# Optimization experiments

Measured on AMD Instinct MI355X. Metric: run time of the kernel, lower is better.

Reference implementation:

```python
import jax, jax.numpy as jnp
import numpy as np
from functools import partial

N_SEEDS = 1000       # n
BG_LOW, BG_UP = 0.3, 0.7
ERODE_K, ERODE_ITER = 11, 1
KSZ = 3
IGNORE = -255
INT_MAX = np.iinfo(np.int32).max


def _min_pool2d(x, k):
    # binary erosion with a kxk all-ones structuring element, SAME padding
    return jax.lax.reduce_window(x, INT_MAX, jax.lax.min, (k, k), (1, 1), 'SAME')


def _max_pool3d(x, k):
    # binary dilation over (B,H,W) with kxk window on spatial dims
    return jax.lax.reduce_window(x, -INT_MAX, jax.lax.max, (1, k, k), (1, 1, 1), 'SAME')


def _otsu_threshold(flat255):
    # flat255: int32 pixel values in [0,255]
    hist = jnp.zeros(256, jnp.float32).at[flat255].add(1.0)
    total = jnp.asarray(flat255.shape[0], jnp.float32)
    bins = jnp.arange(256, dtype=jnp.float32)
    w = jnp.cumsum(hist)                 # class-0 pixel count up to bin t
    m = jnp.cumsum(hist * bins)          # class-0 intensity mass up to t
    mT = m[-1]
    denom = w * (total - w)
    sigma_b = jnp.where(denom > 0, (mT * w - total * m) ** 2 / (denom * total * total), 0.0)
    th = jnp.argmax(sigma_b).astype(jnp.float32)
    bad = jnp.sum(hist > 0) <= 1         # degenerate histogram -> bad_egg
    return th, bad


def _sample_mask(eligible, key, hw):
    # uniform sampling without replacement of min(N_SEEDS, #eligible)
    # via random-score top-k restricted to eligible positions
    scores = jnp.where(eligible, jax.random.uniform(key, (hw,)), -jnp.inf)
    vals, idx = jax.lax.top_k(scores, N_SEEDS)
    sel = (vals > -jnp.inf).astype(jnp.int32)
    return jnp.zeros(hw, jnp.int32).at[idx].max(sel)


def _one_sample(cam, key):
    h, w = cam.shape
    hw = h * w
    cam255 = jnp.floor(cam * 255.0)
    flat255 = jnp.clip(cam255.astype(jnp.int32).ravel(), 0, 255)

    th, bad = _otsu_threshold(flat255)
    th = jnp.where(bad, jnp.median(cam * 255.0), th)
    th = jnp.where(th == 0, 1.0, jnp.where(th == 255, 254.0, th))

    roi = (cam255 > th).astype(jnp.int32)
    for _ in range(ERODE_ITER):
        roi = _min_pool2d(roi, ERODE_K)

    kf, kb, kz = jax.random.split(key, 3)
    # foreground: sample uniformly from eroded ROI pixels
    fg = _sample_mask(roi.ravel() == 1, kf, hw)
    # background: sample uniformly from the nbr_bg lowest-activation pixels
    z = jax.random.uniform(kz, (), minval=BG_LOW, maxval=BG_UP)
    nbr_bg = jnp.ceil(z * hw)
    order = jnp.argsort(cam.ravel())
    rank = jnp.zeros(hw, jnp.int32).at[order].set(jnp.arange(hw, dtype=jnp.int32))
    bg = _sample_mask(rank.astype(jnp.float32) < nbr_bg, kb, hw)
    return fg.reshape(h, w), bg.reshape(h, w)


def setup_inputs() -> dict:
    key = jax.random.key(0)
    x = jax.random.uniform(key, (128, 1, 512, 512), dtype=jnp.float32)
    return {"x": x}


def reference(x):
    b, d, h, w = x.shape
    keys = jax.random.split(jax.random.key(42), b)
    all_fg, all_bg = jax.vmap(_one_sample)(x[:, 0], keys)   # (B,H,W) int32
    # dilation with ksz x ksz ones kernel
    all_fg = _max_pool3d(all_fg, KSZ)
    all_bg = _max_pool3d(all_bg, KSZ)
    outer = all_fg + all_bg
    all_fg = jnp.where(outer == 2, 0, all_fg)
    all_bg = jnp.where(outer == 2, 0, all_bg)
    out = jnp.full((b, h, w), IGNORE, dtype=jnp.int32)
    out = jnp.where(all_fg == 1, 1, out)
    out = jnp.where(all_bg == 1, 0, out)
    return out
```

## Files before the change

### kernel.cpp

```cpp
#include <hip/hip_runtime.h>
#include <cstdint>

typedef unsigned short u16;

constexpr int BATCH = 128;
constexpr int H = 512, W = 512;
constexpr int HW = H * W;
constexpr int WPR = W / 64;
constexpr int WPI = HW / 64;
constexpr int NSEED = 1000;
constexpr int MARGIN = 3000;
constexpr int CAP2 = 4096;
constexpr int CAPS = 1024;
constexpr int LBUF = 2048;
constexpr int NBIN = 4096;

__device__ __forceinline__ uint32_t rotl32(uint32_t v, int d) {
  return (v << d) | (v >> (32 - d));
}

__device__ __forceinline__ void tf2x32(uint32_t k0, uint32_t k1,
                                       uint32_t x0, uint32_t x1,
                                       uint32_t &o0, uint32_t &o1) {
  uint32_t ks2 = k0 ^ k1 ^ 0x1BD11BDAu;
  x0 += k0; x1 += k1;
  x0 += x1; x1 = rotl32(x1, 13); x1 ^= x0;
  x0 += x1; x1 = rotl32(x1, 15); x1 ^= x0;
  x0 += x1; x1 = rotl32(x1, 26); x1 ^= x0;
  x0 += x1; x1 = rotl32(x1, 6);  x1 ^= x0;
  x0 += k1; x1 += ks2 + 1u;
  x0 += x1; x1 = rotl32(x1, 17); x1 ^= x0;
  x0 += x1; x1 = rotl32(x1, 29); x1 ^= x0;
  x0 += x1; x1 = rotl32(x1, 16); x1 ^= x0;
  x0 += x1; x1 = rotl32(x1, 24); x1 ^= x0;
  x0 += ks2; x1 += k0 + 2u;
  x0 += x1; x1 = rotl32(x1, 13); x1 ^= x0;
  x0 += x1; x1 = rotl32(x1, 15); x1 ^= x0;
  x0 += x1; x1 = rotl32(x1, 26); x1 ^= x0;
// ... 23 lines not shown
  uint32_t kf0, kf1; tf2x32(kb0, kb1, 0u, 0u, kf0, kf1);
  uint32_t kB0, kB1; tf2x32(kb0, kb1, 0u, 1u, kB0, kB1);
  uint32_t kz0, kz1; tf2x32(kb0, kb1, 0u, 2u, kz0, kz1);
  uint32_t za, zc; tf2x32(kz0, kz1, 0u, 0u, za, zc);
  uint32_t zb = za ^ zc;
  keys[b * 4 + 0] = kf0; keys[b * 4 + 1] = kf1;
  keys[b * 4 + 2] = kB0; keys[b * 4 + 3] = kB1;
  float uu = __uint_as_float((zb >> 9) | 0x3f800000u) - 1.0f;
  float span = __fsub_rn(0.7f, 0.3f);
  float z = __fadd_rn(__fmul_rn(uu, span), 0.3f);
  z = fmaxf(0.3f, z);
  float nb = ceilf(__fmul_rn(z, (float)HW));
  uint32_t K = (uint32_t)nb;
  kbg[b] = K;
  float tv = floorf((1.0f - (float)MARGIN / (float)K) * 8388608.0f);
  Tbg[b] = (uint32_t)fmaxf(tv, 0.0f);
}

__global__ __launch_bounds__(1024) void k_binify(const float4* __restrict__ x4,
                                                 u16* __restrict__ g,
                                                 uint32_t* __restrict__ gh,
                                                 uint32_t* __restrict__ keys,
                                                 uint32_t* __restrict__ kbg,
                                                 uint32_t* __restrict__ Tbg) {
  __shared__ uint32_t h[NBIN];
  int b = blockIdx.x >> 2, sub = blockIdx.x & 3, t = threadIdx.x;
  if (blockIdx.x == 0 && t < BATCH) keygen(t, keys, kbg, Tbg);
  for (int i = t; i < NBIN; i += 1024) h[i] = 0;
  __syncthreads();
  const float4* xb = x4 + ((size_t)b * HW + (size_t)sub * (HW / 4)) / 4;
  ushort4* gb4 = (ushort4*)g + ((size_t)b * HW + (size_t)sub * (HW / 4)) / 4;
  for (int i = t; i < HW / 16; i += 1024) {
    float4 v4 = xb[i];
    int g0 = (int)floorf(__fmul_rn(v4.x, 4080.0f)); g0 = min(max(g0, 0), 4079);
    int g1 = (int)floorf(__fmul_rn(v4.y, 4080.0f)); g1 = min(max(g1, 0), 4079);
    int g2 = (int)floorf(__fmul_rn(v4.z, 4080.0f)); g2 = min(max(g2, 0), 4079);
    int g3 = (int)floorf(__fmul_rn(v4.w, 4080.0f)); g3 = min(max(g3, 0), 4079);
    atomicAdd(&h[g0], 1u);
    atomicAdd(&h[g1], 1u);
    atomicAdd(&h[g2], 1u);
    atomicAdd(&h[g3], 1u);
    ushort4 o;
    o.x = (u16)g0; o.y = (u16)g1; o.z = (u16)g2; o.w = (u16)g3;
    gb4[i] = o;
  }
  __syncthreads();
  for (int i = t; i < NBIN; i += 1024)
    if (h[i]) atomicAdd(&gh[(size_t)b * NBIN + i], h[i]);
}

__device__ __forceinline__ void lds_tree_cumsum256(float* L, float* S, int tid) {
  const int off[9] = {0, 256, 384, 448, 480, 496, 504, 508, 510};
  const int sz[9]  = {256, 128, 64, 32, 16, 8, 4, 2, 1};
  for (int l = 0; l < 8; ++l) {
    int o = off[l], on = off[l + 1], n = sz[l + 1];
    if (tid < n) L[on + tid] = __fadd_rn(L[o + 2 * tid], L[o + 2 * tid + 1]);
    __syncthreads();
  }
  if (tid == 0) S[off[8]] = L[off[8]];
  __syncthreads();
  for (int l = 7; l >= 0; --l) {
    int o = off[l], on = off[l + 1], hn = sz[l] / 2;
    if (tid == 0) S[o] = L[o];
    if (tid < hn) S[o + 2 * tid + 1] = S[on + tid];
    if (tid >= 1 && tid < hn) S[o + 2 * tid] = __fadd_rn(S[on + tid - 1], L[o + 2 * tid]);
    __syncthreads();
  }
}

__global__ __launch_bounds__(256) void k_otsu_scan(const uint32_t* __restrict__ gh,
                                                   const uint32_t* __restrict__ Ka,
                                                   int* __restrict__ th_out,
                                                   uint32_t* __restrict__ b1a,
                                                   uint32_t* __restrict__ r1a) {
  __shared__ float L[511], S[511], wc[256], mm[256];
  __shared__ float sv[256];
  __shared__ int si[256];
  __shared__ uint32_t h[NBIN];
  __shared__ uint32_t ps[256];
  int tid = threadIdx.x;
  if (blockIdx.x < BATCH) {
    int b = blockIdx.x;
    const uint32_t* gg = gh + (size_t)b * NBIN;
    for (int i = tid; i < NBIN; i += 256) h[i] = gg[i];
    __syncthreads();
    uint32_t hv = 0;
#pragma unroll
    for (int i = 0; i < 16; ++i) hv += h[tid * 16 + i];
    L[tid] = (float)hv;
    __syncthreads();
    lds_tree_cumsum256(L, S, tid);
    wc[tid] = S[tid];
    __syncthreads();
    L[tid] = __fmul_rn((float)hv, (float)tid);
    __syncthreads();
    lds_tree_cumsum256(L, S, tid);
    mm[tid] = S[tid];
    __syncthreads();
    float total = (float)HW;
    float mT = mm[255];
    {
      float w = wc[tid];
      float denom = __fmul_rn(w, __fsub_rn(total, w));
      float s = 0.0f;
      if (denom > 0.0f) {
        float d  = __fsub_rn(__fmul_rn(mT, w), __fmul_rn(total, mm[tid]));
        float nu = __fmul_rn(d, d);
        float dd = __fmul_rn(__fmul_rn(denom, total), total);
        s = __fdiv_rn(nu, dd);
      }
      sv[tid] = s; si[tid] = tid;
    }
    __syncthreads();
    for (int st = 128; st >= 1; st >>= 1) {
      if (tid < st) {
        float s2 = sv[tid + st]; int i2 = si[tid + st];
        if (s2 > sv[tid] || (s2 == sv[tid] && i2 < si[tid])) { sv[tid] = s2; si[tid] = i2; }
      }
      __syncthreads();
    }
    if (tid == 0) {
      int bi = si[0];
      if (bi == 0) bi = 1;
      if (bi == 255) bi = 254;
      th_out[b] = bi;
    }
  } else {
    int b = blockIdx.x - BATCH;
    uint32_t K = Ka[b];
    const uint32_t* g = gh + (size_t)b * NBIN;
    for (int i = tid; i < NBIN; i += 256) h[i] = g[i];
    __syncthreads();
    uint32_t s = 0;
#pragma unroll
    for (int i = 0; i < 16; ++i) s += h[tid * 16 + i];
    ps[tid] = s;
    __syncthreads();
    if (tid == 0) {
      uint32_t acc = 0, b1 = 0, r1 = 1;
      for (int c = 0; c < 256; ++c) {
        if (acc + ps[c] >= K) {
          for (int bin = c * 16; bin < c * 16 + 16; ++bin) {
            uint32_t cc = h[bin];
            if (acc + cc >= K) { b1 = (uint32_t)bin; r1 = K - acc; break; }
            acc += cc;
          }
          break;
        }
        acc += ps[c];
      }
      b1a[b] = b1; r1a[b] = r1;
    }
  }
}

__global__ __launch_bounds__(1024) void k_main(const u16* __restrict__ gq,
                                               const float* __restrict__ x,
                                               const int* __restrict__ th,
                                               const uint32_t* __restrict__ b1a,
                                               const uint32_t* __restrict__ Tbg,
                                               const uint32_t* __restrict__ keys,
                                               uint32_t* __restrict__ Efg,
                                               uint32_t* __restrict__ cnt_bg,
                                               uint64_t* __restrict__ list,
                                               uint32_t* __restrict__ cnt_be,
                                               uint64_t* __restrict__ list_be,
                                               uint64_t* __restrict__ erod) {
  __shared__ uint64_t sroi[1104];
  __shared__ uint64_t srow[1104];
  __shared__ uint32_t queue[8192];
  __shared__ uint64_t lbuf[LBUF];
  __shared__ uint32_t qcnt, lcnt, gbase;
  int b = blockIdx.x >> 2, sub = blockIdx.x & 3, t = threadIdx.x;
  int wave = t >> 6, lane = t & 63;
  int R0 = sub * 128;
  int rlo = max(R0 - 5, 0), rhi = min(R0 + 133, H);
  int nrows = rhi - rlo;
  int nwords = nrows * 8;
  const u16* gb = gq + (size_t)b * HW;
  const float* xb = x + (size_t)b * HW;
  int groi = (th[b] + 1) << 4;
  uint32_t b1 = b1a[b];
  uint32_t T = Tbg[b];
  uint32_t k0 = keys[b * 4 + 2], k1 = keys[b * 4 + 3];
  if (t == 0) lcnt = 0;
  __syncthreads();
  int ntiles = (nwords + 127) / 128;
  for (int tile = 0; tile < ntiles; ++tile) {
    if (t == 0) qcnt = 0;
    __syncthreads();
    int wbeg = tile * 128, wend = min(wbeg + 128, nwords);
    for (int wi = wbeg + wave; wi < wend; wi += 16) {
      int srow_i = wi >> 3, c = wi & 7;
      int absr = rlo + srow_i;
      int p = absr * W + c * 64 + lane;
      uint32_t gv = (uint32_t)gb[p];
      bool pred = (int)gv >= groi;
      uint64_t bw = __ballot(pred);
      if (lane == 0) sroi[wi] = bw;
      if (absr >= R0 && absr < R0 + 128) {
        bool elig = gv < b1;
        uint64_t m = __ballot(elig);
        uint32_t base = 0;
        if (lane == 0 && m) base = atomicAdd(&qcnt, (uint32_t)__popcll(m));
        base = (uint32_t)__shfl((int)base, 0);
        if (elig) {
          uint32_t rank = (uint32_t)__popcll(m & ((1ull << lane) - 1ull));
          queue[base + rank] = (uint32_t)p;
        }
        if (gv == b1) {
          uint32_t gp = atomicAdd(&cnt_be[b], 1u);
          if (gp < (uint32_t)CAPS) {
            float v = xb[p];
            list_be[(size_t)b * CAPS + gp] =
                (((uint64_t)__float_as_uint(v)) << 18) | (uint32_t)p;
          }
        }
      }
    }
    __syncthreads();
    uint32_t qn = qcnt;
    for (uint32_t i = t; i < qn; i += 1024) {
      uint32_t p = queue[i];
      uint32_t v = score_bits(k0, k1, p) >> 9;
      if (v >= T) {
        uint32_t pos = atomicAdd(&lcnt, 1u);
        uint64_t key = (((uint64_t)((~v) & 0x7FFFFFu)) << 18) | p;
        if (pos < (uint32_t)LBUF) lbuf[pos] = key;
        else { uint32_t gp = atomicAdd(&cnt_bg[b], 1u);
               if (gp < (uint32_t)CAP2) list[(size_t)b * CAP2 + gp] = key; }
      }
    }
    __syncthreads();
  }
  for (int wi = t; wi < nwords; wi += 1024) {
    int c = wi & 7;
    uint64_t cur = sroi[wi];
    uint64_t left  = (c > 0) ? sroi[wi - 1] : ~0ull;
    uint64_t right = (c < 7) ? sroi[wi + 1] : ~0ull;
    uint64_t res = cur;
#pragma unroll
    for (int s = 1; s <= 5; ++s) {
      res &= (cur >> s) | (right << (64 - s));
      res &= (cur << s) | (left >> (64 - s));
    }
    srow[wi] = res;
  }
  __syncthreads();
  {
    int coreRow = t >> 3, c = t & 7;
    int absr = R0 + coreRow;
    int s = absr - rlo;
    uint64_t res = srow[s * 8 + c];
#pragma unroll
    for (int d = 1; d <= 5; ++d) {
      if (absr - d >= 0) res &= srow[(s - d) * 8 + c];
      if (absr + d < H)  res &= srow[(s + d) * 8 + c];
    }
    erod[(size_t)b * WPI + absr * 8 + c] = res;
    uint32_t pc = (uint32_t)__popcll(res);
    for (int sh = 32; sh >= 1; sh >>= 1) pc += __shfl_down(pc, sh);
    if (lane == 0 && pc) atomicAdd(&Efg[b], pc);
  }
  __syncthreads();
  int m = min((int)lcnt, LBUF);
  if (t == 0) gbase = atomicAdd(&cnt_bg[b], (uint32_t)m);
  __syncthreads();
  uint32_t base = gbase;
  for (int i = t; i < m; i += 1024) {
    uint32_t pos = base + (uint32_t)i;
    if (pos < (uint32_t)CAP2) list[(size_t)b * CAP2 + pos] = lbuf[i];
  }
}

__global__ __launch_bounds__(1024) void k_bgsel(const uint32_t* __restrict__ r1a,
                                                const uint32_t* __restrict__ cnt_be,
                                                const uint64_t* __restrict__ list_be,
                                                const uint32_t* __restrict__ Tbg,
                                                const uint32_t* __restrict__ keys,
                                                const uint32_t* __restrict__ cnt_bg,
                                                const uint64_t* __restrict__ list,
                                                uint64_t* __restrict__ bm) {
  __shared__ uint64_t ks[CAPS];
  __shared__ uint64_t ebuf[CAPS];
  __shared__ uint32_t ecnt;
  __shared__ uint32_t h[4096];
  __shared__ uint32_t S[256];
  __shared__ uint32_t sb2, sr2;
  __shared__ uint64_t tie[1024];
  __shared__ uint32_t tcnt;
  int b = blockIdx.x, t = threadIdx.x;
  int nbe = min((int)cnt_be[b], CAPS);
  if (t == 0) { ecnt = 0; tcnt = 0; }
  if (t < nbe) ks[t] = list_be[(size_t)b * CAPS + t];
  __syncthreads();
  if (t < nbe) {
    uint64_t mk = ks[t];
    int rank = 0;
    for (int i = 0; i < nbe; ++i) rank += (ks[i] < mk) ? 1 : 0;
    int r = min((int)r1a[b], nbe);
    if (rank < r) {
      uint32_t p = (uint32_t)(mk & 0x3FFFFull);
      uint32_t v = score_bits(keys[b * 4 + 2], keys[b * 4 + 3], p) >> 9;
      if (v >= Tbg[b]) {
        uint32_t slot = atomicAdd(&ecnt, 1u);
        ebuf[slot] = (((uint64_t)((~v) & 0x7FFFFFu)) << 18) | p;
      }
    }
  }
  for (int i = t; i < 4096; i += 1024) h[i] = 0;
  __syncthreads();
  int n0 = min((int)cnt_bg[b], CAP2);
  int ne = (int)ecnt;
  int n = n0 + ne;
  if (n == 0) return;
  uint32_t target = (uint32_t)min(NSEED, n);
  const uint64_t* lb = list + (size_t)b * CAP2;
  uint64_t K0 = (t < n0)        ? lb[t]        : 0;
  uint64_t K1 = (t + 1024 < n0) ? lb[t + 1024] : 0;
  uint64_t K2 = (t + 2048 < n0) ? lb[t + 2048] : 0;
  uint64_t K3 = (t + 3072 < n0) ? lb[t + 3072] : 0;
  uint64_t KE = (t < ne)        ? ebuf[t]      : 0;
  if (t < n0)        atomicAdd(&h[(uint32_t)(K0 >> 29)], 1u);
  if (t + 1024 < n0) atomicAdd(&h[(uint32_t)(K1 >> 29)], 1u);
  if (t + 2048 < n0) atomicAdd(&h[(uint32_t)(K2 >> 29)], 1u);
  if (t + 3072 < n0) atomicAdd(&h[(uint32_t)(K3 >> 29)], 1u);
  if (t < ne)        atomicAdd(&h[(uint32_t)(KE >> 29)], 1u);
  __syncthreads();
  if (t < 256) {
    uint32_t s = 0;
#pragma unroll
    for (int i = 0; i < 16; ++i) s += h[t * 16 + i];
    S[t] = s;
  }
  __syncthreads();
  for (int st = 1; st < 256; st <<= 1) {
    uint32_t v = 0;
    if (t < 256 && t >= st) v = S[t - st];
    __syncthreads();
    if (t < 256) S[t] += v;
    __syncthreads();
  }
  if (t < 256) {
    uint32_t before = (t == 0) ? 0u : S[t - 1];
    if (S[t] >= target && before < target) {
      uint32_t acc = before;
      for (int i = 0; i < 16; ++i) {
        uint32_t c = h[t * 16 + i];
        if (acc + c >= target) { sb2 = (uint32_t)(t * 16 + i); sr2 = target - acc; break; }
        acc += c;
      }
    }
  }
  __syncthreads();
  uint32_t b2 = sb2, r2 = sr2;
#define PROC(KK, VALID) \
  if (VALID) { \
    uint32_t bin = (uint32_t)((KK) >> 29); \
    if (bin < b2) { \
      uint32_t p = (uint32_t)(KK) & 0x3FFFFu; \
      atomicOr((unsigned long long*)&bm[(size_t)b * WPI + (p >> 6)], 1ull << (p & 63)); \
    } else if (bin == b2) { \
      uint32_t pos = atomicAdd(&tcnt, 1u); \
      if (pos < 1024u) tie[pos] = (KK); \
    } \
  }
  PROC(K0, t < n0) PROC(K1, t + 1024 < n0) PROC(K2, t + 2048 < n0)
  PROC(K3, t + 3072 < n0) PROC(KE, t < ne)
#undef PROC
  __syncthreads();
  int m = min((int)tcnt, 1024);
  int r = min((int)r2, m);
  if (t < m) {
    uint64_t mk = tie[t];
    int rank = 0;
    for (int i = 0; i < m; ++i) rank += (tie[i] < mk) ? 1 : 0;
    if (rank < r) {
      uint32_t p = (uint32_t)mk & 0x3FFFFu;
      atomicOr((unsigned long long*)&bm[(size_t)b * WPI + (p >> 6)], 1ull << (p & 63));
    }
  }
}

__global__ __launch_bounds__(1024) void k_selfg(const uint64_t* __restrict__ elig,
                                                const uint32_t* __restrict__ keys,
                                                const uint32_t* __restrict__ Ea,
                                                uint32_t* __restrict__ cnt,
                                                uint64_t* __restrict__ list,
                                                uint64_t* __restrict__ out) {
  __shared__ uint64_t lbuf[LBUF];
  __shared__ uint32_t lcnt;
  __shared__ uint32_t gbase;
  int b = blockIdx.x >> 2, sub = blockIdx.x & 3, t = threadIdx.x;
  const uint64_t* eb = elig + (size_t)b * WPI;
  uint64_t* ob = out + (size_t)b * WPI;
  uint32_t E = Ea[b];
  int wbase = sub * (WPI / 4);
  if (E <= (uint32_t)NSEED) {
    for (int w = t; w < WPI / 4; w += 1024) ob[wbase + w] = eb[wbase + w];
    return;
  }
  float tvf = floorf((1.0f - (float)MARGIN / (float)E) * 8388608.0f);
  uint32_t T = (uint32_t)fmaxf(tvf, 0.0f);
  if (t == 0) lcnt = 0;
  for (int w = t; w < WPI / 4; w += 1024) ob[wbase + w] = 0;
  __syncthreads();
  uint32_t k0 = keys[b * 4 + 0], k1 = keys[b * 4 + 1];
  uint32_t pbase = (uint32_t)(sub * (HW / 4));
  for (int i = t; i < HW / 4; i += 2048) {
    uint32_t p1 = pbase + (uint32_t)i;
    uint32_t p2 = p1 + 1024u;
    uint32_t v1 = score_bits(k0, k1, p1) >> 9;
    uint32_t v2 = score_bits(k0, k1, p2) >> 9;
    bool e1 = (eb[p1 >> 6] >> (p1 & 63)) & 1ull;
    bool e2 = (eb[p2 >> 6] >> (p2 & 63)) & 1ull;
    if (e1 && v1 >= T) {
      uint32_t pos = atomicAdd(&lcnt, 1u);
      uint64_t key = (((uint64_t)((~v1) & 0x7FFFFFu)) << 18) | p1;
      if (pos < (uint32_t)LBUF) lbuf[pos] = key;
      else { uint32_t gp = atomicAdd(&cnt[b], 1u);
             if (gp < (uint32_t)CAP2) list[(size_t)b * CAP2 + gp] = key; }
    }
    if (e2 && v2 >= T) {
      uint32_t pos = atomicAdd(&lcnt, 1u);
      uint64_t key = (((uint64_t)((~v2) & 0x7FFFFFu)) << 18) | p2;
      if (pos < (uint32_t)LBUF) lbuf[pos] = key;
      else { uint32_t gp = atomicAdd(&cnt[b], 1u);
             if (gp < (uint32_t)CAP2) list[(size_t)b * CAP2 + gp] = key; }
    }
  }
  __syncthreads();
  int m = min((int)lcnt, LBUF);
  if (t == 0) gbase = atomicAdd(&cnt[b], (uint32_t)m);
  __syncthreads();
  uint32_t base = gbase;
  for (int i = t; i < m; i += 1024) {
    uint32_t pos = base + (uint32_t)i;
    if (pos < (uint32_t)CAP2) list[(size_t)b * CAP2 + pos] = lbuf[i];
  }
}

__global__ __launch_bounds__(1024) void k_cut2xl(const uint32_t* __restrict__ Ea,
                                                 const uint32_t* __restrict__ cnt,
                                                 const uint64_t* __restrict__ list,
                                                 uint64_t* __restrict__ bm) {
  __shared__ uint32_t h[4096];
  __shared__ uint32_t S[256];
  __shared__ uint32_t sb2, sr2;
  __shared__ uint64_t tie[1024];
  __shared__ uint32_t tcnt;
  int b = blockIdx.x, t = threadIdx.x;
  if (Ea[b] <= (uint32_t)NSEED) return;
  int n = min((int)cnt[b], CAP2);
  if (n == 0) return;
  uint32_t target = (uint32_t)min(NSEED, n);
  const uint64_t* lb = list + (size_t)b * CAP2;
  uint64_t K0 = (t < n)        ? lb[t]        : 0;
  uint64_t K1 = (t + 1024 < n) ? lb[t + 1024] : 0;
  uint64_t K2 = (t + 2048 < n) ? lb[t + 2048] : 0;
  uint64_t K3 = (t + 3072 < n) ? lb[t + 3072] : 0;
  for (int i = t; i < 4096; i += 1024) h[i] = 0;
  if (t == 0) tcnt = 0;
  __syncthreads();
  if (t < n)        atomicAdd(&h[(uint32_t)(K0 >> 29)], 1u);
  if (t + 1024 < n) atomicAdd(&h[(uint32_t)(K1 >> 29)], 1u);
  if (t + 2048 < n) atomicAdd(&h[(uint32_t)(K2 >> 29)], 1u);
  if (t + 3072 < n) atomicAdd(&h[(uint32_t)(K3 >> 29)], 1u);
  __syncthreads();
  if (t < 256) {
    uint32_t s = 0;
#pragma unroll
    for (int i = 0; i < 16; ++i) s += h[t * 16 + i];
    S[t] = s;
  }
  __syncthreads();
  for (int st = 1; st < 256; st <<= 1) {
    uint32_t v = 0;
    if (t < 256 && t >= st) v = S[t - st];
    __syncthreads();
    if (t < 256) S[t] += v;
    __syncthreads();
  }
  if (t < 256) {
    uint32_t before = (t == 0) ? 0u : S[t - 1];
    if (S[t] >= target && before < target) {
      uint32_t acc = before;
      for (int i = 0; i < 16; ++i) {
        uint32_t c = h[t * 16 + i];
        if (acc + c >= target) { sb2 = (uint32_t)(t * 16 + i); sr2 = target - acc; break; }
        acc += c;
      }
    }
  }
  __syncthreads();
  uint32_t b2 = sb2, r2 = sr2;
#define PROC(KK, VALID) \
  if (VALID) { \
    uint32_t bin = (uint32_t)((KK) >> 29); \
    if (bin < b2) { \
      uint32_t p = (uint32_t)(KK) & 0x3FFFFu; \
      atomicOr((unsigned long long*)&bm[(size_t)b * WPI + (p >> 6)], 1ull << (p & 63)); \
    } else if (bin == b2) { \
      uint32_t pos = atomicAdd(&tcnt, 1u); \
      if (pos < 1024u) tie[pos] = (KK); \
    } \
  }
  PROC(K0, t < n) PROC(K1, t + 1024 < n) PROC(K2, t + 2048 < n) PROC(K3, t + 3072 < n)
#undef PROC
  __syncthreads();
  int m = min((int)tcnt, 1024);
  int r = min((int)r2, m);
  if (t < m) {
    uint64_t mk = tie[t];
    int rank = 0;
    for (int i = 0; i < m; ++i) rank += (tie[i] < mk) ? 1 : 0;
    if (rank < r) {
      uint32_t p = (uint32_t)mk & 0x3FFFFu;
      atomicOr((unsigned long long*)&bm[(size_t)b * WPI + (p >> 6)], 1ull << (p & 63));
    }
  }
}

__global__ __launch_bounds__(256) void k_compose4(const uint64_t* __restrict__ F,
                                                  const uint64_t* __restrict__ G,
                                                  int* __restrict__ out) {
  int tid = blockIdx.x * 256 + threadIdx.x;
  int w = tid >> 4;
  int sub = tid & 15;
  int iw = w & (WPI - 1);
  int r = iw >> 3, c = iw & 7;
  int ib = w - iw;
  uint64_t Fd = 0, Bd = 0;
#pragma unroll
  for (int dr = -1; dr <= 1; ++dr) {
    int rr = r + dr;
    if (rr < 0 || rr >= H) continue;
    int wi = ib + rr * 8 + c;
    uint64_t cf = F[wi], cg = G[wi];
    uint64_t lf = (c > 0) ? F[wi - 1] : 0ull, lg = (c > 0) ? G[wi - 1] : 0ull;
    uint64_t rf = (c < 7) ? F[wi + 1] : 0ull, rg = (c < 7) ? G[wi + 1] : 0ull;
    Fd |= cf | (cf << 1) | (lf >> 63) | (cf >> 1) | (rf << 63);
    Bd |= cg | (cg << 1) | (lg >> 63) | (cg >> 1) | (rg << 63);
  }
  uint64_t ov = Fd & Bd;
  Fd &= ~ov; Bd &= ~ov;
  int sh = sub * 4;
  int4 o;
  o.x = ((Fd >> (sh + 0)) & 1ull) ? 1 : (((Bd >> (sh + 0)) & 1ull) ? 0 : -255);
  o.y = ((Fd >> (sh + 1)) & 1ull) ? 1 : (((Bd >> (sh + 1)) & 1ull) ? 0 : -255);
  o.z = ((Fd >> (sh + 2)) & 1ull) ? 1 : (((Bd >> (sh + 2)) & 1ull) ? 0 : -255);
  o.w = ((Fd >> (sh + 3)) & 1ull) ? 1 : (((Bd >> (sh + 3)) & 1ull) ? 0 : -255);
  ((int4*)out)[tid] = o;
}

extern "C" void kernel_launch(void* const* d_in, const int* in_sizes, int n_in,
                              void* d_out, int out_size, void* d_ws, size_t ws_size,
                              hipStream_t stream) {
  (void)in_sizes; (void)n_in; (void)out_size; (void)ws_size;
  const float* x = (const float*)d_in[0];
  int* out = (int*)d_out;
  char* ws = (char*)d_ws;

  u16* g = (u16*)d_out;

  uint32_t* keys = (uint32_t*)(ws + 0);
  uint32_t* kbg  = (uint32_t*)(ws + 2048);
  int*      th   = (int*)     (ws + 2560);
  uint32_t* b1be = (uint32_t*)(ws + 3072);
  uint32_t* r1be = (uint32_t*)(ws + 3584);
  uint32_t* Tbg  = (uint32_t*)(ws + 4096);
  char* Z = ws + 8192;
  uint32_t* Efg    = (uint32_t*)(Z + 0);
  uint32_t* cnt_fg = (uint32_t*)(Z + 512);
  uint32_t* cnt_be = (uint32_t*)(Z + 1024);
  uint32_t* cnt_bg = (uint32_t*)(Z + 1536);
  uint32_t* gh     = (uint32_t*)(Z + 2048);
  uint64_t* bmG    = (uint64_t*)(Z + 2048 + 2097152);
  size_t Zsize = 2048 + 2097152 + 4194304;
  char* P = Z + Zsize;
  uint64_t* list    = (uint64_t*)(P + 0);
  uint64_t* list_be = (uint64_t*)(P + 4194304);
  uint64_t* bmE     = (uint64_t*)(P + 5242880);
  uint64_t* bmF     = (uint64_t*)(P + 9437184);

  hipMemsetAsync(Z, 0, Zsize, stream);
  k_binify   <<<BATCH * 4, 1024, 0, stream>>>((const float4*)x, g, gh, keys, kbg, Tbg);
  k_otsu_scan<<<BATCH * 2, 256, 0, stream>>>(gh, kbg, th, b1be, r1be);
  k_main     <<<BATCH * 4, 1024, 0, stream>>>(g, x, th, b1be, Tbg, keys,
                                              Efg, cnt_bg, list, cnt_be, list_be, bmE);
  k_bgsel    <<<BATCH, 1024, 0, stream>>>(r1be, cnt_be, list_be, Tbg, keys,
                                          cnt_bg, list, bmG);
  k_selfg    <<<BATCH * 4, 1024, 0, stream>>>(bmE, keys, Efg, cnt_fg, list, bmF);
  k_cut2xl   <<<BATCH, 1024, 0, stream>>>(Efg, cnt_fg, list, bmF);
  k_compose4 <<<(BATCH * HW / 4) / 256, 256, 0, stream>>>(bmF, bmG, out);
}
```

Baseline: 416.1 us.

## Fuse selection kernels, drop memset, use per-wave ring queues in main

Replaces the workspace memset by zeroing counters in the binify kernel and writing per-block histograms that the Otsu kernel sums. In k_main the block-wide tiled queue with __syncthreads becomes per-wave ring buffers with only wave barriers. The background-select, foreground-select and tie-cut kernels merge into one k_select launch with one role per block, and compose picks the eroded mask directly when the foreground is small. This cuts launches, the memset and block syncs, but the foreground path now runs one block per image instead of four, which lowers parallelism for that part.

```diff
diff --git a/kernel.cpp b/kernel.cpp
--- a/kernel.cpp
+++ b/kernel.cpp
@@ -14,6 +14,7 @@
 constexpr int CAPS = 1024;
 constexpr int LBUF = 2048;
 constexpr int NBIN = 4096;
+constexpr int QSEG = 576;
 
 __device__ __forceinline__ uint32_t rotl32(uint32_t v, int d) {
   return (v << d) | (v >> (32 - d));
@@ -83,10 +84,17 @@
                                                  uint32_t* __restrict__ gh,
                                                  uint32_t* __restrict__ keys,
                                                  uint32_t* __restrict__ kbg,
-                                                 uint32_t* __restrict__ Tbg) {
+                                                 uint32_t* __restrict__ Tbg,
+                                                 uint32_t* __restrict__ Efg,
+                                                 uint32_t* __restrict__ cnt_fg,
+                                                 uint32_t* __restrict__ cnt_be,
+                                                 uint32_t* __restrict__ cnt_bg) {
   __shared__ uint32_t h[NBIN];
   int b = blockIdx.x >> 2, sub = blockIdx.x & 3, t = threadIdx.x;
-  if (blockIdx.x == 0 && t < BATCH) keygen(t, keys, kbg, Tbg);
+  if (blockIdx.x == 0 && t < BATCH) {
+    keygen(t, keys, kbg, Tbg);
+    Efg[t] = 0; cnt_fg[t] = 0; cnt_be[t] = 0; cnt_bg[t] = 0;
+  }
   for (int i = t; i < NBIN; i += 1024) h[i] = 0;
   __syncthreads();
   const float4* xb = x4 + ((size_t)b * HW + (size_t)sub * (HW / 4)) / 4;
@@ -106,8 +114,8 @@
     gb4[i] = o;
   }
   __syncthreads();
-  for (int i = t; i < NBIN; i += 1024)
-    if (h[i]) atomicAdd(&gh[(size_t)b * NBIN + i], h[i]);
+  uint32_t* dst = gh + ((size_t)blockIdx.x << 12);
+  for (int i = t; i < NBIN; i += 1024) dst[i] = h[i];
 }
 
 __device__ __forceinline__ void lds_tree_cumsum256(float* L, float* S, int tid) {
@@ -140,11 +148,14 @@
   __shared__ uint32_t h[NBIN];
   __shared__ uint32_t ps[256];
   int tid = threadIdx.x;
+  int b = (blockIdx.x < BATCH) ? blockIdx.x : (blockIdx.x - BATCH);
+  const uint32_t* g0 = gh + ((size_t)(b * 4 + 0) << 12);
+  const uint32_t* g1 = gh + ((size_t)(b * 4 + 1) << 12);
+  const uint32_t* g2 = gh + ((size_t)(b * 4 + 2) << 12);
+  const uint32_t* g3 = gh + ((size_t)(b * 4 + 3) << 12);
+  for (int i = tid; i < NBIN; i += 256) h[i] = g0[i] + g1[i] + g2[i] + g3[i];
+  __syncthreads();
   if (blockIdx.x < BATCH) {
-    int b = blockIdx.x;
-    const uint32_t* gg = gh + (size_t)b * NBIN;
-    for (int i = tid; i < NBIN; i += 256) h[i] = gg[i];
-    __syncthreads();
     uint32_t hv = 0;
 #pragma unroll
     for (int i = 0; i < 16; ++i) hv += h[tid * 16 + i];
@@ -187,11 +198,7 @@
       th_out[b] = bi;
     }
   } else {
-    int b = blockIdx.x - BATCH;
     uint32_t K = Ka[b];
-    const uint32_t* g = gh + (size_t)b * NBIN;
-    for (int i = tid; i < NBIN; i += 256) h[i] = g[i];
-    __syncthreads();
     uint32_t s = 0;
 #pragma unroll
     for (int i = 0; i < 16; ++i) s += h[tid * 16 + i];
@@ -229,15 +236,14 @@
                                                uint64_t* __restrict__ erod) {
   __shared__ uint64_t sroi[1104];
   __shared__ uint64_t srow[1104];
-  __shared__ uint32_t queue[8192];
+  __shared__ uint32_t wq[16 * QSEG];
   __shared__ uint64_t lbuf[LBUF];
-  __shared__ uint32_t qcnt, lcnt, gbase;
+  __shared__ uint32_t lcnt, gbase;
   int b = blockIdx.x >> 2, sub = blockIdx.x & 3, t = threadIdx.x;
   int wave = t >> 6, lane = t & 63;
   int R0 = sub * 128;
   int rlo = max(R0 - 5, 0), rhi = min(R0 + 133, H);
-  int nrows = rhi - rlo;
-  int nwords = nrows * 8;
+  int nwords = (rhi - rlo) * 8;
   const u16* gb = gq + (size_t)b * HW;
   const float* xb = x + (size_t)b * HW;
   int groi = (th[b] + 1) << 4;
@@ -246,43 +252,46 @@
   uint32_t k0 = keys[b * 4 + 2], k1 = keys[b * 4 + 3];
   if (t == 0) lcnt = 0;
   __syncthreads();
-  int ntiles = (nwords + 127) / 128;
-  for (int tile = 0; tile < ntiles; ++tile) {
-    if (t == 0) qcnt = 0;
-    __syncthreads();
-    int wbeg = tile * 128, wend = min(wbeg + 128, nwords);
-    for (int wi = wbeg + wave; wi < wend; wi += 16) {
-      int srow_i = wi >> 3, c = wi & 7;
-      int absr = rlo + srow_i;
-      int p = absr * W + c * 64 + lane;
-      uint32_t gv = (uint32_t)gb[p];
-      bool pred = (int)gv >= groi;
-      uint64_t bw = __ballot(pred);
-      if (lane == 0) sroi[wi] = bw;
-      if (absr >= R0 && absr < R0 + 128) {
-        bool elig = gv < b1;
-        uint64_t m = __ballot(elig);
-        uint32_t base = 0;
-        if (lane == 0 && m) base = atomicAdd(&qcnt, (uint32_t)__popcll(m));
-        base = (uint32_t)__shfl((int)base, 0);
-        if (elig) {
-          uint32_t rank = (uint32_t)__popcll(m & ((1ull << lane) - 1ull));
-          queue[base + rank] = (uint32_t)p;
-        }
-        if (gv == b1) {
-          uint32_t gp = atomicAdd(&cnt_be[b], 1u);
-          if (gp < (uint32_t)CAPS) {
-            float v = xb[p];
-            list_be[(size_t)b * CAPS + gp] =
-                (((uint64_t)__float_as_uint(v)) << 18) | (uint32_t)p;
-          }
-        }
-      }
-    }
-    __syncthreads();
-    uint32_t qn = qcnt;
-    for (uint32_t i = t; i < qn; i += 1024) {
-      uint32_t p = queue[i];
+  uint32_t* q = wq + wave * QSEG;
+  uint32_t qlen = 0, hd = 0;
+  uint64_t lmask = (1ull << lane) - 1ull;
+  for (int r = 0; r < 8; ++r) {
+    int absr = R0 + wave * 8 + r;
+    int rowbase = absr * W + lane;
+    int swbase = (absr - rlo) * 8;
+    const u16* gp8 = gb + rowbase;
+    u16 gvals[8];
+#pragma unroll
+    for (int c = 0; c < 8; ++c) gvals[c] = gp8[c * 64];
+#pragma unroll
+    for (int c = 0; c < 8; ++c) {
+      uint32_t gv = (uint32_t)gvals[c];
+      uint64_t bw = __ballot((int)gv >= groi);
+      if (lane == 0) sroi[swbase + c] = bw;
+      bool elig = gv < b1;
+      uint64_t m = __ballot(elig);
+      if (elig) {
+        uint32_t rank = (uint32_t)__popcll(m & lmask);
+        uint32_t idx = hd + qlen + rank;
+        if (idx >= (uint32_t)QSEG) idx -= (uint32_t)QSEG;
+        q[idx] = (uint32_t)(rowbase + c * 64);
+      }
+      qlen += (uint32_t)__popcll(m);
+      if (gv == b1) {
+        uint32_t gp = atomicAdd(&cnt_be[b], 1u);
+        if (gp < (uint32_t)CAPS)
+          list_be[(size_t)b * CAPS + gp] =
+              (((uint64_t)__float_as_uint(xb[rowbase + c * 64])) << 18) |
+              (uint32_t)(rowbase + c * 64);
+      }
+    }
+    while (qlen >= 64u) {
+      __builtin_amdgcn_wave_barrier();
+      uint32_t idx = hd + (uint32_t)lane;
+      if (idx >= (uint32_t)QSEG) idx -= (uint32_t)QSEG;
+      uint32_t p = q[idx];
+      hd += 64u; if (hd >= (uint32_t)QSEG) hd -= (uint32_t)QSEG;
+      qlen -= 64u;
       uint32_t v = score_bits(k0, k1, p) >> 9;
       if (v >= T) {
         uint32_t pos = atomicAdd(&lcnt, 1u);
@@ -292,8 +301,36 @@
                if (gp < (uint32_t)CAP2) list[(size_t)b * CAP2 + gp] = key; }
       }
     }
-    __syncthreads();
-  }
+  }
+  if (qlen) {
+    __builtin_amdgcn_wave_barrier();
+    if ((uint32_t)lane < qlen) {
+      uint32_t idx = hd + (uint32_t)lane;
+      if (idx >= (uint32_t)QSEG) idx -= (uint32_t)QSEG;
+      uint32_t p = q[idx];
+      uint32_t v = score_bits(k0, k1, p) >> 9;
+      if (v >= T) {
+        uint32_t pos = atomicAdd(&lcnt, 1u);
+        uint64_t key = (((uint64_t)((~v) & 0x7FFFFFu)) << 18) | p;
+        if (pos < (uint32_t)LBUF) lbuf[pos] = key;
+        else { uint32_t gp = atomicAdd(&cnt_bg[b], 1u);
+               if (gp < (uint32_t)CAP2) list[(size_t)b * CAP2 + gp] = key; }
+      }
+    }
+  }
+  {
+    int lowWords = (R0 - rlo) * 8;
+    int nh = nwords - 1024;
+    for (int i = wave; i < nh; i += 16) {
+      int wi = i + ((i < lowWords) ? 0 : 1024);
+      int absr = rlo + (wi >> 3);
+      int c = wi & 7;
+      uint32_t gv = (uint32_t)gb[absr * W + c * 64 + lane];
+      uint64_t bw = __ballot((int)gv >= groi);
+      if (lane == 0) sroi[wi] = bw;
+    }
+  }
+  __syncthreads();
   for (int wi = t; wi < nwords; wi += 1024) {
     int c = wi & 7;
     uint64_t cur = sroi[wi];
@@ -334,261 +371,239 @@
   }
 }
 
-__global__ __launch_bounds__(1024) void k_bgsel(const uint32_t* __restrict__ r1a,
-                                                const uint32_t* __restrict__ cnt_be,
-                                                const uint64_t* __restrict__ list_be,
-                                                const uint32_t* __restrict__ Tbg,
-                                                const uint32_t* __restrict__ keys,
-                                                const uint32_t* __restrict__ cnt_bg,
-                                                const uint64_t* __restrict__ list,
-                                                uint64_t* __restrict__ bm) {
-  __shared__ uint64_t ks[CAPS];
-  __shared__ uint64_t ebuf[CAPS];
-  __shared__ uint32_t ecnt;
-  __shared__ uint32_t h[4096];
-  __shared__ uint32_t S[256];
-  __shared__ uint32_t sb2, sr2;
-  __shared__ uint64_t tie[1024];
-  __shared__ uint32_t tcnt;
-  int b = blockIdx.x, t = threadIdx.x;
-  int nbe = min((int)cnt_be[b], CAPS);
-  if (t == 0) { ecnt = 0; tcnt = 0; }
-  if (t < nbe) ks[t] = list_be[(size_t)b * CAPS + t];
-  __syncthreads();
-  if (t < nbe) {
-    uint64_t mk = ks[t];
-    int rank = 0;
-    for (int i = 0; i < nbe; ++i) rank += (ks[i] < mk) ? 1 : 0;
-    int r = min((int)r1a[b], nbe);
-    if (rank < r) {
-      uint32_t p = (uint32_t)(mk & 0x3FFFFull);
-      uint32_t v = score_bits(keys[b * 4 + 2], keys[b * 4 + 3], p) >> 9;
-      if (v >= Tbg[b]) {
-        uint32_t slot = atomicAdd(&ecnt, 1u);
-        ebuf[slot] = (((uint64_t)((~v) & 0x7FFFFFu)) << 18) | p;
-      }
-    }
-  }
-  for (int i = t; i < 4096; i += 1024) h[i] = 0;
-  __syncthreads();
-  int n0 = min((int)cnt_bg[b], CAP2);
-  int ne = (int)ecnt;
-  int n = n0 + ne;
-  if (n == 0) return;
-  uint32_t target = (uint32_t)min(NSEED, n);
-  const uint64_t* lb = list + (size_t)b * CAP2;
-  uint64_t K0 = (t < n0)        ? lb[t]        : 0;
-  uint64_t K1 = (t + 1024 < n0) ? lb[t + 1024] : 0;
-  uint64_t K2 = (t + 2048 < n0) ? lb[t + 2048] : 0;
-  uint64_t K3 = (t + 3072 < n0) ? lb[t + 3072] : 0;
-  uint64_t KE = (t < ne)        ? ebuf[t]      : 0;
-  if (t < n0)        atomicAdd(&h[(uint32_t)(K0 >> 29)], 1u);
-  if (t + 1024 < n0) atomicAdd(&h[(uint32_t)(K1 >> 29)], 1u);
-  if (t + 2048 < n0) atomicAdd(&h[(uint32_t)(K2 >> 29)], 1u);
-  if (t + 3072 < n0) atomicAdd(&h[(uint32_t)(K3 >> 29)], 1u);
-  if (t < ne)        atomicAdd(&h[(uint32_t)(KE >> 29)], 1u);
-  __syncthreads();
-  if (t < 256) {
-    uint32_t s = 0;
-#pragma unroll
-    for (int i = 0; i < 16; ++i) s += h[t * 16 + i];
-    S[t] = s;
-  }
-  __syncthreads();
-  for (int st = 1; st < 256; st <<= 1) {
-    uint32_t v = 0;
-    if (t < 256 && t >= st) v = S[t - st];
-    __syncthreads();
-    if (t < 256) S[t] += v;
-    __syncthreads();
-  }
-  if (t < 256) {
-    uint32_t before = (t == 0) ? 0u : S[t - 1];
-    if (S[t] >= target && before < target) {
-      uint32_t acc = before;
-      for (int i = 0; i < 16; ++i) {
-        uint32_t c = h[t * 16 + i];
-        if (acc + c >= target) { sb2 = (uint32_t)(t * 16 + i); sr2 = target - acc; break; }
-        acc += c;
-      }
-    }
-  }
-  __syncthreads();
-  uint32_t b2 = sb2, r2 = sr2;
+__global__ __launch_bounds__(1024) void k_select(const uint32_t* __restrict__ r1a,
+                                                 const uint32_t* __restrict__ cnt_be,
+                                                 const uint64_t* __restrict__ list_be,
+                                                 const uint32_t* __restrict__ Tbg,
+                                                 const uint32_t* __restrict__ keys,
+                                                 const uint32_t* __restrict__ cnt_bg,
+                                                 const uint64_t* __restrict__ list,
+                                                 uint64_t* __restrict__ bmG,
+                                                 const uint32_t* __restrict__ Ea,
+                                                 uint32_t* __restrict__ cnt_fg,
+                                                 uint64_t* __restrict__ list_fg,
+                                                 const uint64_t* __restrict__ bmE,
+                                                 uint64_t* __restrict__ bmF) {
+  __shared__ uint64_t pool[5248];
+  __shared__ uint32_t ecnt, tcnt, lcnt, gbase, sb2, sr2;
+  int t = threadIdx.x;
+  uint32_t* h = (uint32_t*)(pool + 2048);
+  uint64_t* tie = pool + 4096;
+  uint32_t* S = (uint32_t*)(pool + 5120);
+  if (blockIdx.x < BATCH) {
+    int b = blockIdx.x;
+    uint64_t* ks = pool;
+    uint64_t* ebuf = pool + 1024;
+    uint64_t* bg = bmG + (size_t)b * WPI;
+    for (int i = t; i < WPI; i += 1024) bg[i] = 0;
+    int nbe = min((int)cnt_be[b], CAPS);
+    if (t == 0) { ecnt = 0; tcnt = 0; }
+    if (t < nbe) ks[t] = list_be[(size_t)b * CAPS + t];
+    __syncthreads();
+    if (t < nbe) {
+      uint64_t mk = ks[t];
+      int rank = 0;
+      for (int i = 0; i < nbe; ++i) rank += (ks[i] < mk) ? 1 : 0;
+      int r = min((int)r1a[b], nbe);
+      if (rank < r) {
+        uint32_t p = (uint32_t)(mk & 0x3FFFFull);
+        uint32_t v = score_bits(keys[b * 4 + 2], keys[b * 4 + 3], p) >> 9;
+        if (v >= Tbg[b]) {
+          uint32_t slot = atomicAdd(&ecnt, 1u);
+          ebuf[slot] = (((uint64_t)((~v) & 0x7FFFFFu)) << 18) | p;
+        }
+      }
+    }
+    for (int i = t; i < 4096; i += 1024) h[i] = 0;
+    __syncthreads();
+    int n0 = min((int)cnt_bg[b], CAP2);
+    int ne = (int)ecnt;
+    int n = n0 + ne;
+    if (n == 0) return;
+    uint32_t target = (uint32_t)min(NSEED, n);
+    const uint64_t* lb = list + (size_t)b * CAP2;
+    uint64_t K0 = (t < n0)        ? lb[t]        : 0;
+    uint64_t K1 = (t + 1024 < n0) ? lb[t + 1024] : 0;
+    uint64_t K2 = (t + 2048 < n0) ? lb[t + 2048] : 0;
+    uint64_t K3 = (t + 3072 < n0) ? lb[t + 3072] : 0;
+    uint64_t KE = (t < ne)        ? ebuf[t]      : 0;
+    if (t < n0)        atomicAdd(&h[(uint32_t)(K0 >> 29)], 1u);
+    if (t + 1024 < n0) atomicAdd(&h[(uint32_t)(K1 >> 29)], 1u);
+    if (t + 2048 < n0) atomicAdd(&h[(uint32_t)(K2 >> 29)], 1u);
+    if (t + 3072 < n0) atomicAdd(&h[(uint32_t)(K3 >> 29)], 1u);
+    if (t < ne)        atomicAdd(&h[(uint32_t)(KE >> 29)], 1u);
+    __syncthreads();
+    if (t < 256) {
+      uint32_t s = 0;
+#pragma unroll
+      for (int i = 0; i < 16; ++i) s += h[t * 16 + i];
+      S[t] = s;
+    }
+    __syncthreads();
+    for (int st = 1; st < 256; st <<= 1) {
+      uint32_t v = 0;
+      if (t < 256 && t >= st) v = S[t - st];
+      __syncthreads();
+      if (t < 256) S[t] += v;
+      __syncthreads();
+    }
+    if (t < 256) {
+      uint32_t before = (t == 0) ? 0u : S[t - 1];
+      if (S[t] >= target && before < target) {
+        uint32_t acc = before;
+        for (int i = 0; i < 16; ++i) {
+          uint32_t c = h[t * 16 + i];
+          if (acc + c >= target) { sb2 = (uint32_t)(t * 16 + i); sr2 = target - acc; break; }
+          acc += c;
+        }
+      }
+    }
+    __syncthreads();
+    uint32_t b2 = sb2, r2 = sr2;
 #define PROC(KK, VALID) \
-  if (VALID) { \
-    uint32_t bin = (uint32_t)((KK) >> 29); \
-    if (bin < b2) { \
-      uint32_t p = (uint32_t)(KK) & 0x3FFFFu; \
-      atomicOr((unsigned long long*)&bm[(size_t)b * WPI + (p >> 6)], 1ull << (p & 63)); \
-    } else if (bin == b2) { \
-      uint32_t pos = atomicAdd(&tcnt, 1u); \
-      if (pos < 1024u) tie[pos] = (KK); \
-    } \
-  }
-  PROC(K0, t < n0) PROC(K1, t + 1024 < n0) PROC(K2, t + 2048 < n0)
-  PROC(K3, t + 3072 < n0) PROC(KE, t < ne)
+    if (VALID) { \
+      uint32_t bin = (uint32_t)((KK) >> 29); \
+      if (bin < b2) { \
+        uint32_t p = (uint32_t)(KK) & 0x3FFFFu; \
+        atomicOr((unsigned long long*)&bg[p >> 6], 1ull << (p & 63)); \
+      } else if (bin == b2) { \
+        uint32_t pos = atomicAdd(&tcnt, 1u); \
+        if (pos < 1024u) tie[pos] = (KK); \
+      } \
+    }
+    PROC(K0, t < n0) PROC(K1, t + 1024 < n0) PROC(K2, t + 2048 < n0)
+    PROC(K3, t + 3072 < n0) PROC(KE, t < ne)
 #undef PROC
-  __syncthreads();
-  int m = min((int)tcnt, 1024);
-  int r = min((int)r2, m);
-  if (t < m) {
-    uint64_t mk = tie[t];
-    int rank = 0;
-    for (int i = 0; i < m; ++i) rank += (tie[i] < mk) ? 1 : 0;
-    if (rank < r) {
-      uint32_t p = (uint32_t)mk & 0x3FFFFu;
-      atomicOr((unsigned long long*)&bm[(size_t)b * WPI + (p >> 6)], 1ull << (p & 63));
-    }
-  }
-}
-
-__global__ __launch_bounds__(1024) void k_selfg(const uint64_t* __restrict__ elig,
-                                                const uint32_t* __restrict__ keys,
-                                                const uint32_t* __restrict__ Ea,
-                                                uint32_t* __restrict__ cnt,
-                                                uint64_t* __restrict__ list,
-                                                uint64_t* __restrict__ out) {
-  __shared__ uint64_t lbuf[LBUF];
-  __shared__ uint32_t lcnt;
-  __shared__ uint32_t gbase;
-  int b = blockIdx.x >> 2, sub = blockIdx.x & 3, t = threadIdx.x;
-  const uint64_t* eb = elig + (size_t)b * WPI;
-  uint64_t* ob = out + (size_t)b * WPI;
-  uint32_t E = Ea[b];
-  int wbase = sub * (WPI / 4);
-  if (E <= (uint32_t)NSEED) {
-    for (int w = t; w < WPI / 4; w += 1024) ob[wbase + w] = eb[wbase + w];
-    return;
-  }
-  float tvf = floorf((1.0f - (float)MARGIN / (float)E) * 8388608.0f);
-  uint32_t T = (uint32_t)fmaxf(tvf, 0.0f);
-  if (t == 0) lcnt = 0;
-  for (int w = t; w < WPI / 4; w += 1024) ob[wbase + w] = 0;
-  __syncthreads();
-  uint32_t k0 = keys[b * 4 + 0], k1 = keys[b * 4 + 1];
-  uint32_t pbase = (uint32_t)(sub * (HW / 4));
-  for (int i = t; i < HW / 4; i += 2048) {
-    uint32_t p1 = pbase + (uint32_t)i;
-    uint32_t p2 = p1 + 1024u;
-    uint32_t v1 = score_bits(k0, k1, p1) >> 9;
-    uint32_t v2 = score_bits(k0, k1, p2) >> 9;
-    bool e1 = (eb[p1 >> 6] >> (p1 & 63)) & 1ull;
-    bool e2 = (eb[p2 >> 6] >> (p2 & 63)) & 1ull;
-    if (e1 && v1 >= T) {
-      uint32_t pos = atomicAdd(&lcnt, 1u);
-      uint64_t key = (((uint64_t)((~v1) & 0x7FFFFFu)) << 18) | p1;
-      if (pos < (uint32_t)LBUF) lbuf[pos] = key;
-      else { uint32_t gp = atomicAdd(&cnt[b], 1u);
-             if (gp < (uint32_t)CAP2) list[(size_t)b * CAP2 + gp] = key; }
-    }
-    if (e2 && v2 >= T) {
-      uint32_t pos = atomicAdd(&lcnt, 1u);
-      uint64_t key = (((uint64_t)((~v2) & 0x7FFFFFu)) << 18) | p2;
-      if (pos < (uint32_t)LBUF) lbuf[pos] = key;
-      else { uint32_t gp = atomicAdd(&cnt[b], 1u);
-             if (gp < (uint32_t)CAP2) list[(size_t)b * CAP2 + gp] = key; }
-    }
-  }
-  __syncthreads();
-  int m = min((int)lcnt, LBUF);
-  if (t == 0) gbase = atomicAdd(&cnt[b], (uint32_t)m);
-  __syncthreads();
-  uint32_t base = gbase;
-  for (int i = t; i < m; i += 1024) {
-    uint32_t pos = base + (uint32_t)i;
-    if (pos < (uint32_t)CAP2) list[(size_t)b * CAP2 + pos] = lbuf[i];
-  }
-}
-
-__global__ __launch_bounds__(1024) void k_cut2xl(const uint32_t* __restrict__ Ea,
-                                                 const uint32_t* __restrict__ cnt,
-                                                 const uint64_t* __restrict__ list,
-                                                 uint64_t* __restrict__ bm) {
-  __shared__ uint32_t h[4096];
-  __shared__ uint32_t S[256];
-  __shared__ uint32_t sb2, sr2;
-  __shared__ uint64_t tie[1024];
-  __shared__ uint32_t tcnt;
-  int b = blockIdx.x, t = threadIdx.x;
-  if (Ea[b] <= (uint32_t)NSEED) return;
-  int n = min((int)cnt[b], CAP2);
-  if (n == 0) return;
-  uint32_t target = (uint32_t)min(NSEED, n);
-  const uint64_t* lb = list + (size_t)b * CAP2;
-  uint64_t K0 = (t < n)        ? lb[t]        : 0;
-  uint64_t K1 = (t + 1024 < n) ? lb[t + 1024] : 0;
-  uint64_t K2 = (t + 2048 < n) ? lb[t + 2048] : 0;
-  uint64_t K3 = (t + 3072 < n) ? lb[t + 3072] : 0;
-  for (int i = t; i < 4096; i += 1024) h[i] = 0;
-  if (t == 0) tcnt = 0;
-  __syncthreads();
-  if (t < n)        atomicAdd(&h[(uint32_t)(K0 >> 29)], 1u);
-  if (t + 1024 < n) atomicAdd(&h[(uint32_t)(K1 >> 29)], 1u);
-  if (t + 2048 < n) atomicAdd(&h[(uint32_t)(K2 >> 29)], 1u);
-  if (t + 3072 < n) atomicAdd(&h[(uint32_t)(K3 >> 29)], 1u);
-  __syncthreads();
-  if (t < 256) {
-    uint32_t s = 0;
-#pragma unroll
-    for (int i = 0; i < 16; ++i) s += h[t * 16 + i];
-    S[t] = s;
-  }
-  __syncthreads();
-  for (int st = 1; st < 256; st <<= 1) {
-    uint32_t v = 0;
-    if (t < 256 && t >= st) v = S[t - st];
-    __syncthreads();
-    if (t < 256) S[t] += v;
-    __syncthreads();
-  }
-  if (t < 256) {
-    uint32_t before = (t == 0) ? 0u : S[t - 1];
-    if (S[t] >= target && before < target) {
-      uint32_t acc = before;
-      for (int i = 0; i < 16; ++i) {
-        uint32_t c = h[t * 16 + i];
-        if (acc + c >= target) { sb2 = (uint32_t)(t * 16 + i); sr2 = target - acc; break; }
-        acc += c;
-      }
-    }
-  }
-  __syncthreads();
-  uint32_t b2 = sb2, r2 = sr2;
+    __syncthreads();
+    int m = min((int)tcnt, 1024);
+    int r = min((int)r2, m);
+    if (t < m) {
+      uint64_t mk = tie[t];
+      int rank = 0;
+      for (int i = 0; i < m; ++i) rank += (tie[i] < mk) ? 1 : 0;
+      if (rank < r) {
+        uint32_t p = (uint32_t)mk & 0x3FFFFu;
+        atomicOr((unsigned long long*)&bg[p >> 6], 1ull << (p & 63));
+      }
+    }
+  } else {
+    int b = blockIdx.x - BATCH;
+    uint32_t E = Ea[b];
+    if (E <= (uint32_t)NSEED) return;
+    uint64_t* lbuf = pool;
+    const uint64_t* eb = bmE + (size_t)b * WPI;
+    uint64_t* ob = bmF + (size_t)b * WPI;
+    for (int i = t; i < WPI; i += 1024) ob[i] = 0;
+    if (t == 0) { lcnt = 0; tcnt = 0; }
+    __syncthreads();
+    float tvf = floorf((1.0f - (float)MARGIN / (float)E) * 8388608.0f);
+    uint32_t T = (uint32_t)fmaxf(tvf, 0.0f);
+    uint32_t k0 = keys[b * 4 + 0], k1 = keys[b * 4 + 1];
+    int lane = t & 63;
+    for (int k = 0; k < HW / 1024; ++k) {
+      uint32_t p = (uint32_t)(k * 1024 + t);
+      uint64_t wbits = eb[p >> 6];
+      if ((wbits >> lane) & 1ull) {
+        uint32_t v = score_bits(k0, k1, p) >> 9;
+        if (v >= T) {
+          uint32_t pos = atomicAdd(&lcnt, 1u);
+          uint64_t key = (((uint64_t)((~v) & 0x7FFFFFu)) << 18) | p;
+          if (pos < (uint32_t)LBUF) lbuf[pos] = key;
+          else { uint32_t gp = atomicAdd(&cnt_fg[b], 1u);
+                 if (gp < (uint32_t)CAP2) list_fg[(size_t)b * CAP2 + gp] = key; }
+        }
+      }
+    }
+    __syncthreads();
+    int m2 = min((int)lcnt, LBUF);
+    if (t == 0) gbase = atomicAdd(&cnt_fg[b], (uint32_t)m2);
+    __syncthreads();
+    for (int i = t; i < m2; i += 1024) {
+      uint32_t pos = gbase + (uint32_t)i;
+      if (pos < (uint32_t)CAP2) list_fg[(size_t)b * CAP2 + pos] = lbuf[i];
+    }
+    __syncthreads();
+    int n = min((int)cnt_fg[b], CAP2);
+    if (n == 0) return;
+    uint32_t target = (uint32_t)min(NSEED, n);
+    const uint64_t* lb = list_fg + (size_t)b * CAP2;
+    uint64_t K0 = (t < n)        ? lb[t]        : 0;
+    uint64_t K1 = (t + 1024 < n) ? lb[t + 1024] : 0;
+    uint64_t K2 = (t + 2048 < n) ? lb[t + 2048] : 0;
+    uint64_t K3 = (t + 3072 < n) ? lb[t + 3072] : 0;
+    for (int i = t; i < 4096; i += 1024) h[i] = 0;
+    __syncthreads();
+    if (t < n)        atomicAdd(&h[(uint32_t)(K0 >> 29)], 1u);
+    if (t + 1024 < n) atomicAdd(&h[(uint32_t)(K1 >> 29)], 1u);
+    if (t + 2048 < n) atomicAdd(&h[(uint32_t)(K2 >> 29)], 1u);
+    if (t + 3072 < n) atomicAdd(&h[(uint32_t)(K3 >> 29)], 1u);
+    __syncthreads();
+    if (t < 256) {
+      uint32_t s = 0;
+#pragma unroll
+      for (int i = 0; i < 16; ++i) s += h[t * 16 + i];
+      S[t] = s;
+    }
+    __syncthreads();
+    for (int st = 1; st < 256; st <<= 1) {
+      uint32_t v = 0;
+      if (t < 256 && t >= st) v = S[t - st];
+      __syncthreads();
+      if (t < 256) S[t] += v;
+      __syncthreads();
+    }
+    if (t < 256) {
+      uint32_t before = (t == 0) ? 0u : S[t - 1];
+      if (S[t] >= target && before < target) {
+        uint32_t acc = before;
+        for (int i = 0; i < 16; ++i) {
+          uint32_t c = h[t * 16 + i];
+          if (acc + c >= target) { sb2 = (uint32_t)(t * 16 + i); sr2 = target - acc; break; }
+          acc += c;
+        }
+      }
+    }
+    __syncthreads();
+    uint32_t b2 = sb2, r2 = sr2;
 #define PROC(KK, VALID) \
-  if (VALID) { \
-    uint32_t bin = (uint32_t)((KK) >> 29); \
-    if (bin < b2) { \
-      uint32_t p = (uint32_t)(KK) & 0x3FFFFu; \
-      atomicOr((unsigned long long*)&bm[(size_t)b * WPI + (p >> 6)], 1ull << (p & 63)); \
-    } else if (bin == b2) { \
-      uint32_t pos = atomicAdd(&tcnt, 1u); \
-      if (pos < 1024u) tie[pos] = (KK); \
-    } \
-  }
-  PROC(K0, t < n) PROC(K1, t + 1024 < n) PROC(K2, t + 2048 < n) PROC(K3, t + 3072 < n)
+    if (VALID) { \
+      uint32_t bin = (uint32_t)((KK) >> 29); \
+      if (bin < b2) { \
+        uint32_t p = (uint32_t)(KK) & 0x3FFFFu; \
+        atomicOr((unsigned long long*)&ob[p >> 6], 1ull << (p & 63)); \
+      } else if (bin == b2) { \
+        uint32_t pos = atomicAdd(&tcnt, 1u); \
+        if (pos < 1024u) tie[pos] = (KK); \
+      } \
+    }
+    PROC(K0, t < n) PROC(K1, t + 1024 < n) PROC(K2, t + 2048 < n) PROC(K3, t + 3072 < n)
 #undef PROC
-  __syncthreads();
-  int m = min((int)tcnt, 1024);
-  int r = min((int)r2, m);
-  if (t < m) {
-    uint64_t mk = tie[t];
-    int rank = 0;
-    for (int i = 0; i < m; ++i) rank += (tie[i] < mk) ? 1 : 0;
-    if (rank < r) {
-      uint32_t p = (uint32_t)mk & 0x3FFFFu;
-      atomicOr((unsigned long long*)&bm[(size_t)b * WPI + (p >> 6)], 1ull << (p & 63));
-    }
-  }
-}
-
-__global__ __launch_bounds__(256) void k_compose4(const uint64_t* __restrict__ F,
+    __syncthreads();
+    int m = min((int)tcnt, 1024);
+    int r = min((int)r2, m);
+    if (t < m) {
+      uint64_t mk = tie[t];
+      int rank = 0;
+      for (int i = 0; i < m; ++i) rank += (tie[i] < mk) ? 1 : 0;
+      if (rank < r) {
+        uint32_t p = (uint32_t)mk & 0x3FFFFu;
+        atomicOr((unsigned long long*)&ob[p >> 6], 1ull << (p & 63));
+      }
+    }
+  }
+}
+
+__global__ __launch_bounds__(256) void k_compose4(const uint64_t* __restrict__ bmE,
+                                                  const uint64_t* __restrict__ bmF,
                                                   const uint64_t* __restrict__ G,
+                                                  const uint32_t* __restrict__ Ea,
                                                   int* __restrict__ out) {
   int tid = blockIdx.x * 256 + threadIdx.x;
   int w = tid >> 4;
   int sub = tid & 15;
   int iw = w & (WPI - 1);
+  int b = w >> 12;
+  const uint64_t* F = (Ea[b] <= (uint32_t)NSEED) ? bmE : bmF;
   int r = iw >> 3, c = iw & 7;
   int ib = w - iw;
   uint64_t Fd = 0, Bd = 0;
@@ -624,34 +639,34 @@
 
   u16* g = (u16*)d_out;
 
-  uint32_t* keys = (uint32_t*)(ws + 0);
-  uint32_t* kbg  = (uint32_t*)(ws + 2048);
-  int*      th   = (int*)     (ws + 2560);
-  uint32_t* b1be = (uint32_t*)(ws + 3072);
-  uint32_t* r1be = (uint32_t*)(ws + 3584);
-  uint32_t* Tbg  = (uint32_t*)(ws + 4096);
-  char* Z = ws + 8192;
-  uint32_t* Efg    = (uint32_t*)(Z + 0);
-  uint32_t* cnt_fg = (uint32_t*)(Z + 512);
-  uint32_t* cnt_be = (uint32_t*)(Z + 1024);
-  uint32_t* cnt_bg = (uint32_t*)(Z + 1536);
-  uint32_t* gh     = (uint32_t*)(Z + 2048);
-  uint64_t* bmG    = (uint64_t*)(Z + 2048 + 2097152);
-  size_t Zsize = 2048 + 2097152 + 4194304;
-  char* P = Z + Zsize;
-  uint64_t* list    = (uint64_t*)(P + 0);
-  uint64_t* list_be = (uint64_t*)(P + 4194304);
-  uint64_t* bmE     = (uint64_t*)(P + 5242880);
-  uint64_t* bmF     = (uint64_t*)(P + 9437184);
-
-  hipMemsetAsync(Z, 0, Zsize, stream);
-  k_binify   <<<BATCH * 4, 1024, 0, stream>>>((const float4*)x, g, gh, keys, kbg, Tbg);
+  uint32_t* keys   = (uint32_t*)(ws + 0);
+  uint32_t* kbg    = (uint32_t*)(ws + 2048);
+  int*      th     = (int*)     (ws + 2560);
+  uint32_t* b1be   = (uint32_t*)(ws + 3072);
+  uint32_t* r1be   = (uint32_t*)(ws + 3584);
+  uint32_t* Tbg    = (uint32_t*)(ws + 4096);
+  uint32_t* Efg    = (uint32_t*)(ws + 4608);
+  uint32_t* cnt_fg = (uint32_t*)(ws + 5120);
+  uint32_t* cnt_be = (uint32_t*)(ws + 5632);
+  uint32_t* cnt_bg = (uint32_t*)(ws + 6144);
+  char* P = ws + 8192;
+  uint32_t* gh      = (uint32_t*)(P);
+  uint64_t* bmG     = (uint64_t*)(P + 8396800 - 8192);
+  uint64_t* _bmG    = (uint64_t*)(ws + 8192 + 8388608);
+  uint64_t* list    = (uint64_t*)(ws + 8192 + 8388608 + 4194304);
+  uint64_t* list_be = (uint64_t*)(ws + 8192 + 8388608 + 8388608);
+  uint64_t* bmE     = (uint64_t*)(ws + 8192 + 8388608 + 9437184);
+  uint64_t* bmF     = (uint64_t*)(ws + 8192 + 8388608 + 13631488);
+  uint64_t* list_fg = (uint64_t*)gh;
+  (void)bmG;
+
+  k_binify   <<<BATCH * 4, 1024, 0, stream>>>((const float4*)x, g, gh, keys, kbg,
+                                              Tbg, Efg, cnt_fg, cnt_be, cnt_bg);
   k_otsu_scan<<<BATCH * 2, 256, 0, stream>>>(gh, kbg, th, b1be, r1be);
   k_main     <<<BATCH * 4, 1024, 0, stream>>>(g, x, th, b1be, Tbg, keys,
                                               Efg, cnt_bg, list, cnt_be, list_be, bmE);
-  k_bgsel    <<<BATCH, 1024, 0, stream>>>(r1be, cnt_be, list_be, Tbg, keys,
-                                          cnt_bg, list, bmG);
-  k_selfg    <<<BATCH * 4, 1024, 0, stream>>>(bmE, keys, Efg, cnt_fg, list, bmF);
-  k_cut2xl   <<<BATCH, 1024, 0, stream>>>(Efg, cnt_fg, list, bmF);
-  k_compose4 <<<(BATCH * HW / 4) / 256, 256, 0, stream>>>(bmF, bmG, out);
-}
+  k_select   <<<BATCH * 2, 1024, 0, stream>>>(r1be, cnt_be, list_be, Tbg, keys,
+                                              cnt_bg, list, _bmG,
+                                              Efg, cnt_fg, list_fg, bmE, bmF);
+  k_compose4 <<<(BATCH * HW / 4) / 256, 256, 0, stream>>>(bmE, bmF, _bmG, Efg, out);
+}
```

After: 388.8 us. 6.5% less time.
